# Optimization experiments

Hardware: AMD Instinct MI355X
Metric: run time of the kernel (lower is better)

The kernel has to match this reference:

```python
import jax, jax.numpy as jnp
import numpy as np

B, S, E = 2, 2049, 512
H, WIN = 8, 1024
D = E // H


def setup_inputs() -> dict:
    key = jax.random.key(0)
    ks = jax.random.split(key, 11)
    sc = 0.02
    return {
        "x": jax.random.normal(ks[0], (B, S, E), dtype=jnp.float32),
        "Wq": jax.random.normal(ks[1], (E, E), dtype=jnp.float32) * sc,
        "bq": jnp.zeros((E,), dtype=jnp.float32),
        "Wk": jax.random.normal(ks[2], (E, E), dtype=jnp.float32) * sc,
        "bk": jnp.zeros((E,), dtype=jnp.float32),
        "Wv": jax.random.normal(ks[3], (E, E), dtype=jnp.float32) * sc,
        "bv": jnp.zeros((E,), dtype=jnp.float32),
        "Wo": jax.random.normal(ks[4], (E, E), dtype=jnp.float32) * sc,
        "bo": jnp.zeros((E,), dtype=jnp.float32),
        "w_gate": jax.random.normal(ks[5], (2 * E,), dtype=jnp.float32) * sc,
        "b_gate": jnp.zeros((), dtype=jnp.float32),
    }


def reference(x, Wq, bq, Wk, bk, Wv, bv, Wo, bo, w_gate, b_gate):
    scale = D ** -0.5
    q_flat = x @ Wq + bq  # [B,S,E]
    k_flat = x @ Wk + bk
    v_flat = x @ Wv + bv
    q = q_flat.reshape(B, S, H, D).transpose(0, 2, 1, 3)  # [B,H,S,D]
    k = k_flat.reshape(B, S, H, D).transpose(0, 2, 1, 3)
    v = v_flat.reshape(B, S, H, D).transpose(0, 2, 1, 3)

    scores = jnp.einsum("bhqd,bhkd->bhqk", q, k) * scale  # [B,H,S,S]

    # Gaussian positional bias: -0.5*|i-j|^2/sigma^2, sigma = window/2
    pos = jnp.arange(S)
    dist = jnp.abs(pos[:, None] - pos[None, :]).astype(jnp.float32)
    sigma = WIN / 2.0
    bias = -0.5 * dist ** 2 / (sigma ** 2)  # [S,S]
    scores = scores + bias[None, None]

    # Pairwise gate: sigmoid(concat(q_i,k_j) @ w + b) == sigmoid(q_i.wq + k_j.wk + b)
    gq = q_flat @ w_gate[:E]       # [B,S]
    gk = k_flat @ w_gate[E:]       # [B,S]
    gates = jax.nn.sigmoid(gq[:, :, None] + gk[:, None, :] + b_gate)  # [B,S,S]
    scores = scores * gates[:, None]  # broadcast over heads

    local_mask = jnp.where(dist <= WIN, 0.0, -jnp.inf).astype(jnp.float32)
    scores = scores + local_mask[None, None]

    attn = jax.nn.softmax(scores, axis=-1)
    out = jnp.einsum("bhqk,bhkd->bhqd", attn, v)  # [B,H,S,D]
    out = out.transpose(0, 2, 1, 3).reshape(B, S, E)
    return out @ Wo + bo
```

## Files before the change

### kernel.cpp

```cpp
#include <hip/hip_runtime.h>
#include <cstdint>
#include <cstddef>

#define B_ 2
#define S_ 2049
#define E_ 512
#define H_ 8
#define WIN_ 1024
#define MROWS (B_*S_)
#define SP_ 2176
#define GBUFN 4104

typedef unsigned short ushort_t;
typedef __attribute__((ext_vector_type(8))) short bf16x8;
typedef __attribute__((ext_vector_type(4))) float f32x4;

#define MFMA16(a,b,c) __builtin_amdgcn_mfma_f32_16x16x32_bf16(a,b,c,0,0,0)

__device__ __forceinline__ ushort_t f2bf(float f) {
  unsigned int u = __float_as_uint(f);
  u += 0x7fffu + ((u >> 16) & 1u);
  return (ushort_t)(u >> 16);
}
__device__ __forceinline__ float bf2f(ushort_t h) {
  return __uint_as_float(((unsigned int)h) << 16);
}

__global__ __launch_bounds__(256) void convert_all_kernel(
    const float* __restrict__ x, const float* __restrict__ W0,
    const float* __restrict__ W1, const float* __restrict__ W2,
    const float* __restrict__ W3, ushort_t* __restrict__ xb,
    ushort_t* __restrict__ Wt_all, ushort_t* __restrict__ WoHi)
{
  __shared__ float tile[32][33];
  int bid = blockIdx.x;
  if (bid < 2049) {
    int idx = bid * 256 + threadIdx.x;
    float4 v = ((const float4*)x)[idx];
    ushort4 o;
    o.x = f2bf(v.x); o.y = f2bf(v.y); o.z = f2bf(v.z); o.w = f2bf(v.w);
    ((ushort4*)xb)[idx] = o;
    return;
  }
  int wid = bid - 2049;
  int z = wid >> 8, rem = wid & 255;
  const float* W = (z == 0) ? W0 : (z == 1) ? W1 : (z == 2) ? W2 : W3;
  int k0 = (rem >> 4) * 32, n0 = (rem & 15) * 32;
  int r = threadIdx.x >> 5, c = threadIdx.x & 31;
#pragma unroll
  for (int i = 0; i < 4; ++i) {
    int rr = r + i * 8;
    tile[rr][c] = W[(size_t)(k0 + rr) * E_ + n0 + c];
  }
  __syncthreads();
#pragma unroll
  for (int i = 0; i < 4; ++i) {
    int rr = r + i * 8;
    float v = tile[c][rr];
    size_t dst = (size_t)(n0 + rr) * E_ + k0 + c;
    if (z < 3) Wt_all[(size_t)z * E_ * E_ + dst] = f2bf(v);
    else       WoHi[dst] = f2bf(v);
  }
}

__global__ __launch_bounds__(256) void gemm_qkv_kernel(
    const ushort_t* __restrict__ xb, const ushort_t* __restrict__ Wt_all,
    const float* __restrict__ bq, const float* __restrict__ bk,
    const float* __restrict__ bv, const float* __restrict__ wg,
    ushort_t* __restrict__ qkb, ushort_t* __restrict__ vT,
    float* __restrict__ gq_acc, float* __restrict__ gk_acc)
{
  __shared__ __align__(16) ushort_t As[128][40];
  __shared__ __align__(16) ushort_t Bs[128][40];
  int tid = threadIdx.x;
  int lane = tid & 63, w = tid >> 6;
  int l15 = lane & 15, quad = lane >> 4;
  int wm = (w & 1) * 64, wn = (w >> 1) * 64;
  int z = blockIdx.z;
  const ushort_t* Wt = Wt_all + (size_t)z * E_ * E_;
  const float* bias = (z == 0) ? bq : (z == 1) ? bk : bv;
  int bm = blockIdx.x * 128, bn = blockIdx.y * 128;

  int ar = tid >> 1, ac = (tid & 1) * 16;
  int am = bm + ar; if (am >= MROWS) am = MROWS - 1;
  const ushort_t* ap = xb + (size_t)am * E_ + ac;
  const ushort_t* bp = Wt + (size_t)(bn + ar) * E_ + ac;

  const f32x4 fz = {0.f, 0.f, 0.f, 0.f};
  f32x4 acc[4][4];
#pragma unroll
  for (int mt = 0; mt < 4; ++mt)
#pragma unroll
    for (int nt = 0; nt < 4; ++nt) acc[mt][nt] = fz;

  int4 pa0 = *(const int4*)ap, pa1 = *(const int4*)(ap + 8);
  int4 pb0 = *(const int4*)bp, pb1 = *(const int4*)(bp + 8);

  for (int k0 = 0; k0 < E_; k0 += 32) {
    __syncthreads();
    int kn = (k0 + 32 < E_) ? (k0 + 32) : k0;
    int4 na0 = *(const int4*)(ap + kn), na1 = *(const int4*)(ap + kn + 8);
    int4 nb0 = *(const int4*)(bp + kn), nb1 = *(const int4*)(bp + kn + 8);
    *(int4*)&As[ar][ac] = pa0; *(int4*)&As[ar][ac + 8] = pa1;
    *(int4*)&Bs[ar][ac] = pb0; *(int4*)&Bs[ar][ac + 8] = pb1;
    __syncthreads();
    bf16x8 a[4], bfr[4];
#pragma unroll
    for (int mt = 0; mt < 4; ++mt) a[mt] = *(const bf16x8*)&As[wm + mt * 16 + l15][quad * 8];
#pragma unroll
    for (int nt = 0; nt < 4; ++nt) bfr[nt] = *(const bf16x8*)&Bs[wn + nt * 16 + l15][quad * 8];
#pragma unroll
    for (int mt = 0; mt < 4; ++mt)
#pragma unroll
      for (int nt = 0; nt < 4; ++nt)
        acc[mt][nt] = MFMA16(a[mt], bfr[nt], acc[mt][nt]);
    pa0 = na0; pa1 = na1; pb0 = nb0; pb1 = nb1;
  }

  float bb[4];
#pragma unroll
  for (int nt = 0; nt < 4; ++nt) bb[nt] = bias[bn + wn + nt * 16 + l15];

  if (z < 2) {
    ushort_t* C = qkb + (size_t)z * MROWS * E_;
#pragma unroll
    for (int mt = 0; mt < 4; ++mt)
#pragma unroll
      for (int nt = 0; nt < 4; ++nt)
#pragma unroll
        for (int r = 0; r < 4; ++r) {
          int m = bm + wm + mt * 16 + quad * 4 + r;
          if (m < MROWS)
            C[(size_t)m * E_ + bn + wn + nt * 16 + l15] = f2bf(acc[mt][nt][r] + bb[nt]);
        }
    const float* wgp = wg + (size_t)z * E_;
    float wv[4];
#pragma unroll
    for (int nt = 0; nt < 4; ++nt) wv[nt] = wgp[bn + wn + nt * 16 + l15];
    float* gacc = (z == 0) ? gq_acc : gk_acc;
#pragma unroll
    for (int mt = 0; mt < 4; ++mt)
#pragma unroll
      for (int r = 0; r < 4; ++r) {
        float s = 0.f;
#pragma unroll
        for (int nt = 0; nt < 4; ++nt) s = fmaf(acc[mt][nt][r] + bb[nt], wv[nt], s);
        s += __shfl_xor(s, 1, 16); s += __shfl_xor(s, 2, 16);
        s += __shfl_xor(s, 4, 16); s += __shfl_xor(s, 8, 16);
        int m = bm + wm + mt * 16 + quad * 4 + r;
        if (l15 == 0 && m < MROWS) atomicAdd(&gacc[m], s);
      }
  } else {
#pragma unroll
    for (int mt = 0; mt < 4; ++mt)
#pragma unroll
      for (int nt = 0; nt < 4; ++nt) {
        int dg = bn + wn + nt * 16 + l15;
        int h = dg >> 6, d = dg & 63;
#pragma unroll
        for (int r = 0; r < 4; ++r) {
          int m = bm + wm + mt * 16 + quad * 4 + r;
          if (m < MROWS) {
            int b = (m >= S_) ? 1 : 0;
            int i = m - b * S_;
            vT[((size_t)(b * H_ + h) * 64 + d) * SP_ + i] = f2bf(acc[mt][nt][r] + bb[nt]);
          }
        }
      }
  }
}

__global__ __launch_bounds__(256) void attn_kernel(
    const ushort_t* __restrict__ qb, const ushort_t* __restrict__ kb,
    const ushort_t* __restrict__ vT, const float* __restrict__ gq_raw,
    const float* __restrict__ gk_raw, const float* __restrict__ bgate,
    ushort_t* __restrict__ ahi, ushort_t* __restrict__ alo)
{
  __shared__ __align__(16) ushort_t Ks[64][72];
  __shared__ __align__(16) ushort_t Vt[64][72];
  __shared__ __align__(16) ushort_t Ps[4][16][72];
  __shared__ float lls[4][16];
  __shared__ float gbs[2176];

  int tid = threadIdx.x;
  int lane = tid & 63, w = tid >> 6;
  int l15 = lane & 15, quad = lane >> 4;

  int bh = blockIdx.x & 15;
  int qidx = blockIdx.x >> 4;
  int off = (qidx + 1) >> 1;
  int qt = 16 + ((qidx & 1) ? -off : off);
  int h = bh & 7, b = bh >> 3;
  int i0 = qt * 64;
  const float coef = -0.5f / (512.f * 512.f);

  int i = i0 + w * 16 + l15;
  int ic = (i < S_) ? i : S_ - 1;
  bf16x8 qf0 = *(const bf16x8*)&qb[((size_t)(b * S_ + ic)) * E_ + h * 64 + quad * 8];
  bf16x8 qf1 = *(const bf16x8*)&qb[((size_t)(b * S_ + ic)) * E_ + h * 64 + 32 + quad * 8];
#pragma unroll
  for (int e = 0; e < 8; ++e) {
    qf0[e] = (short)f2bf(bf2f((ushort_t)qf0[e]) * 0.125f);
    qf1[e] = (short)f2bf(bf2f((ushort_t)qf1[e]) * 0.125f);
  }
  float av = __expf(-(gq_raw[b * S_ + ic] + bgate[0]));
  float fdi = (i < S_) ? (float)i : -1e5f;

  int jlo = i0 - WIN_; if (jlo < 0) jlo = 0;
  int jt_lo = jlo >> 6;
  int jhi = i0 + 63 + WIN_; if (jhi > S_ - 1) jhi = S_ - 1;
  int jt_hi = jhi >> 6;
  int jbase = jt_lo << 6;
  int nwin = (jt_hi - jt_lo + 1) << 6;

  for (int tt = tid; tt < nwin; tt += 256) {
    int j = jbase + tt; int jc = (j < S_) ? j : S_ - 1;
    gbs[tt] = __expf(-gk_raw[b * S_ + jc]);
  }

  int srow = tid >> 2, scol = (tid & 3) * 16;
  const ushort_t* kb_base = kb + (size_t)b * S_ * E_ + h * 64 + scol;
  const ushort_t* vb_base = vT + ((size_t)(b * H_ + h) * 64 + srow) * SP_ + scol;

  int4 ka0, ka1, va0, va1;
  {
    int jc0 = jbase + srow; if (jc0 > S_ - 1) jc0 = S_ - 1;
    const int4* kp = (const int4*)(kb_base + (size_t)jc0 * E_);
    ka0 = kp[0]; ka1 = kp[1];
    const int4* vp = (const int4*)(vb_base + jbase);
    va0 = vp[0]; va1 = vp[1];
  }

  const f32x4 fz = {0.f, 0.f, 0.f, 0.f};
  f32x4 Ov[4] = {fz, fz, fz, fz};
  float l_run = 0.f;

  for (int jt = jt_lo; jt <= jt_hi; ++jt) {
    int j0 = jt << 6;
    __syncthreads();
    int jn = (jt < jt_hi) ? ((jt + 1) << 6) : j0;
    int jcn = jn + srow; if (jcn > S_ - 1) jcn = S_ - 1;
    const int4* kp = (const int4*)(kb_base + (size_t)jcn * E_);
    int4 nk0 = kp[0], nk1 = kp[1];
    const int4* vp = (const int4*)(vb_base + jn);
    int4 nv0 = vp[0], nv1 = vp[1];
    *(int4*)&Ks[srow][scol]     = ka0; *(int4*)&Ks[srow][scol + 8] = ka1;
    *(int4*)&Vt[srow][scol]     = va0; *(int4*)&Vt[srow][scol + 8] = va1;
    __syncthreads();

    f32x4 st[4];
#pragma unroll
    for (int nt = 0; nt < 4; ++nt) {
      bf16x8 kf0 = *(const bf16x8*)&Ks[nt * 16 + l15][quad * 8];
      bf16x8 kf1 = *(const bf16x8*)&Ks[nt * 16 + l15][32 + quad * 8];
      f32x4 s = MFMA16(kf0, qf0, fz);
      st[nt] = MFMA16(kf1, qf1, s);
    }

    bool full = ((j0 + 63 - i0) <= WIN_) && ((i0 + 63 - j0) <= WIN_)
                && (j0 + 63 < S_) && (i0 + 63 < S_);
    float ps = 0.f;
    float jq = (float)(j0 + quad * 4);
    if (full) {
#pragma unroll
      for (int nt = 0; nt < 4; ++nt) {
        f32x4 g4 = *(const f32x4*)&gbs[(j0 - jbase) + nt * 16 + quad * 4];
#pragma unroll
        for (int r = 0; r < 4; ++r) {
          float f = fdi - (jq + (float)(nt * 16 + r));
          float gate = __builtin_amdgcn_rcpf(fmaf(av, g4[r], 1.f));
          float p = __expf(fmaf(f * f, coef, st[nt][r]) * gate);
          st[nt][r] = p; ps += p;
        }
      }
    } else {
#pragma unroll
      for (int nt = 0; nt < 4; ++nt) {
        f32x4 g4 = *(const f32x4*)&gbs[(j0 - jbase) + nt * 16 + quad * 4];
#pragma unroll
        for (int r = 0; r < 4; ++r) {
          int j = j0 + nt * 16 + quad * 4 + r;
          float fj = (j < S_) ? (float)j : 1e5f;
          float f = fdi - fj;
          float gate = __builtin_amdgcn_rcpf(fmaf(av, g4[r], 1.f));
          float t = fmaf(f * f, coef, st[nt][r]) * gate;
          t = (__builtin_fabsf(f) <= 1024.f) ? t : -1e30f;
          float p = __expf(t);
          st[nt][r] = p; ps += p;
        }
      }
    }
    ps += __shfl_xor(ps, 16);
    ps += __shfl_xor(ps, 32);
    l_run += ps;

#pragma unroll
    for (int nt = 0; nt < 4; ++nt) {
      uint2 pk;
      pk.x = (unsigned int)f2bf(st[nt][0]) | ((unsigned int)f2bf(st[nt][1]) << 16);
      pk.y = (unsigned int)f2bf(st[nt][2]) | ((unsigned int)f2bf(st[nt][3]) << 16);
      *(uint2*)&Ps[w][l15][nt * 16 + quad * 4] = pk;
    }
    bf16x8 p0 = *(const bf16x8*)&Ps[w][l15][quad * 8];
    bf16x8 p1 = *(const bf16x8*)&Ps[w][l15][32 + quad * 8];
#pragma unroll
    for (int nt = 0; nt < 4; ++nt) {
      bf16x8 v0 = *(const bf16x8*)&Vt[nt * 16 + l15][quad * 8];
      bf16x8 v1 = *(const bf16x8*)&Vt[nt * 16 + l15][32 + quad * 8];
      Ov[nt] = MFMA16(p0, v0, Ov[nt]);
      Ov[nt] = MFMA16(p1, v1, Ov[nt]);
    }
    ka0 = nk0; ka1 = nk1; va0 = nv0; va1 = nv1;
  }

  if (lane < 16) lls[w][lane] = 1.f / l_run;
  f32x4 inv4 = *(const f32x4*)&lls[w][quad * 4];
#pragma unroll
  for (int r = 0; r < 4; ++r) {
    int irow = i0 + w * 16 + quad * 4 + r;
    if (irow < S_) {
#pragma unroll
      for (int nt = 0; nt < 4; ++nt) {
        float o = Ov[nt][r] * inv4[r];
        ushort_t hv = f2bf(o);
        size_t idx = ((size_t)(b * S_ + irow)) * E_ + h * 64 + nt * 16 + l15;
        ahi[idx] = hv;
        alo[idx] = f2bf(o - bf2f(hv));
      }
    }
  }
}

__global__ __launch_bounds__(256) void gemm_out_kernel(
    const ushort_t* __restrict__ Ahi, const ushort_t* __restrict__ Alo,
    const ushort_t* __restrict__ Whi, const float* __restrict__ bias,
    float* __restrict__ C)
{
  __shared__ __align__(16) ushort_t AsH[64][40];
  __shared__ __align__(16) ushort_t AsL[64][40];
  __shared__ __align__(16) ushort_t BsW[128][40];
  int tid = threadIdx.x;
  int lane = tid & 63, w = tid >> 6;
  int l15 = lane & 15, quad = lane >> 4;
  int wm = (w & 1) * 32, wn = (w >> 1) * 64;
  int bm = blockIdx.x * 64, bn = blockIdx.y * 128;

  int ar = tid >> 2, ac = (tid & 3) * 8;
  int am = bm + ar; if (am >= MROWS) am = MROWS - 1;
  const ushort_t* ahp = Ahi + (size_t)am * E_ + ac;
  const ushort_t* alp = Alo + (size_t)am * E_ + ac;
  int br = tid >> 1, bc = (tid & 1) * 16;
  const ushort_t* bp = Whi + (size_t)(bn + br) * E_ + bc;

  const f32x4 fz = {0.f, 0.f, 0.f, 0.f};
  f32x4 acc[2][4];
#pragma unroll
  for (int mt = 0; mt < 2; ++mt)
#pragma unroll
    for (int nt = 0; nt < 4; ++nt) acc[mt][nt] = fz;

  int4 ph = *(const int4*)ahp, pl = *(const int4*)alp;
  int4 pb0 = *(const int4*)bp, pb1 = *(const int4*)(bp + 8);

  for (int k0 = 0; k0 < E_; k0 += 32) {
    __syncthreads();
    int kn = (k0 + 32 < E_) ? (k0 + 32) : k0;
    int4 nh = *(const int4*)(ahp + kn), nl = *(const int4*)(alp + kn);
    int4 nb0 = *(const int4*)(bp + kn), nb1 = *(const int4*)(bp + kn + 8);
    *(int4*)&AsH[ar][ac] = ph;
    *(int4*)&AsL[ar][ac] = pl;
    *(int4*)&BsW[br][bc] = pb0; *(int4*)&BsW[br][bc + 8] = pb1;
    __syncthreads();
    bf16x8 ah[2], al[2], bw[4];
#pragma unroll
    for (int mt = 0; mt < 2; ++mt) {
      ah[mt] = *(const bf16x8*)&AsH[wm + mt * 16 + l15][quad * 8];
      al[mt] = *(const bf16x8*)&AsL[wm + mt * 16 + l15][quad * 8];
    }
#pragma unroll
    for (int nt = 0; nt < 4; ++nt) bw[nt] = *(const bf16x8*)&BsW[wn + nt * 16 + l15][quad * 8];
#pragma unroll
    for (int mt = 0; mt < 2; ++mt)
#pragma unroll
      for (int nt = 0; nt < 4; ++nt) {
        acc[mt][nt] = MFMA16(ah[mt], bw[nt], acc[mt][nt]);
        acc[mt][nt] = MFMA16(al[mt], bw[nt], acc[mt][nt]);
      }
    ph = nh; pl = nl; pb0 = nb0; pb1 = nb1;
  }
#pragma unroll
  for (int nt = 0; nt < 4; ++nt) {
    float bb = bias[bn + wn + nt * 16 + l15];
#pragma unroll
    for (int mt = 0; mt < 2; ++mt)
#pragma unroll
      for (int r = 0; r < 4; ++r) {
        int m = bm + wm + mt * 16 + quad * 4 + r;
        if (m < MROWS)
          C[(size_t)m * E_ + bn + wn + nt * 16 + l15] = acc[mt][nt][r] + bb;
      }
  }
}

extern "C" void kernel_launch(void* const* d_in, const int* in_sizes, int n_in,
                              void* d_out, int out_size, void* d_ws, size_t ws_size,
                              hipStream_t stream) {
  const float* x  = (const float*)d_in[0];
  const float* Wq = (const float*)d_in[1];
  const float* bq = (const float*)d_in[2];
  const float* Wk = (const float*)d_in[3];
  const float* bk = (const float*)d_in[4];
  const float* Wv = (const float*)d_in[5];
  const float* bv = (const float*)d_in[6];
  const float* Wo = (const float*)d_in[7];
  const float* bo = (const float*)d_in[8];
  const float* wg = (const float*)d_in[9];
  const float* bg = (const float*)d_in[10];

  char* p = (char*)d_ws;
  ushort_t* xb     = (ushort_t*)p; p += (size_t)MROWS * E_ * 2;
  ushort_t* Wt_all = (ushort_t*)p; p += (size_t)3 * E_ * E_ * 2;
  ushort_t* WoHi   = (ushort_t*)p; p += (size_t)E_ * E_ * 2;
  ushort_t* qkb    = (ushort_t*)p; p += (size_t)2 * MROWS * E_ * 2;
  ushort_t* vT     = (ushort_t*)p; p += (size_t)B_ * H_ * 64 * SP_ * 2;
  float*    gq_acc = (float*)p;    p += (size_t)GBUFN * 4;
  float*    gk_acc = (float*)p;    p += (size_t)GBUFN * 4;
  ushort_t* aHi    = (ushort_t*)p; p += (size_t)MROWS * E_ * 2;
  ushort_t* aLo    = (ushort_t*)p; p += (size_t)MROWS * E_ * 2;

  hipMemsetAsync(gq_acc, 0, 2 * (size_t)GBUFN * 4, stream);
  hipLaunchKernelGGL(convert_all_kernel, dim3(3073), dim3(256), 0, stream,
                     x, Wq, Wk, Wv, Wo, xb, Wt_all, WoHi);
  hipLaunchKernelGGL(gemm_qkv_kernel, dim3(33, 4, 3), dim3(256), 0, stream,
                     xb, Wt_all, bq, bk, bv, wg, qkb, vT, gq_acc, gk_acc);
  hipLaunchKernelGGL(attn_kernel, dim3(33 * 16), dim3(256), 0, stream,
                     qkb, qkb + (size_t)MROWS * E_, vT, gq_acc, gk_acc, bg, aHi, aLo);
  hipLaunchKernelGGL(gemm_out_kernel, dim3(65, 4), dim3(256), 0, stream,
                     aHi, aLo, WoHi, bo, (float*)d_out);
}
```

Measured before the change: 177.6 us.

## Split attention key range across two blocks, fuse x conversion into QKV GEMM

```diff
diff --git a/kernel.cpp b/kernel.cpp
--- a/kernel.cpp
+++ b/kernel.cpp
@@ -10,6 +10,8 @@
 #define MROWS (B_*S_)
 #define SP_ 2176
 #define GBUFN 4104
+#define HS_ (H_*S_)
+#define BHS_ (B_*H_*S_)
 
 typedef unsigned short ushort_t;
 typedef __attribute__((ext_vector_type(8))) short bf16x8;
@@ -26,26 +28,15 @@
   return __uint_as_float(((unsigned int)h) << 16);
 }
 
-__global__ __launch_bounds__(256) void convert_all_kernel(
-    const float* __restrict__ x, const float* __restrict__ W0,
-    const float* __restrict__ W1, const float* __restrict__ W2,
-    const float* __restrict__ W3, ushort_t* __restrict__ xb,
+__global__ __launch_bounds__(256) void convert_w_kernel(
+    const float* __restrict__ W0, const float* __restrict__ W1,
+    const float* __restrict__ W2, const float* __restrict__ W3,
     ushort_t* __restrict__ Wt_all, ushort_t* __restrict__ WoHi)
 {
   __shared__ float tile[32][33];
-  int bid = blockIdx.x;
-  if (bid < 2049) {
-    int idx = bid * 256 + threadIdx.x;
-    float4 v = ((const float4*)x)[idx];
-    ushort4 o;
-    o.x = f2bf(v.x); o.y = f2bf(v.y); o.z = f2bf(v.z); o.w = f2bf(v.w);
-    ((ushort4*)xb)[idx] = o;
-    return;
-  }
-  int wid = bid - 2049;
-  int z = wid >> 8, rem = wid & 255;
+  int z = blockIdx.z;
   const float* W = (z == 0) ? W0 : (z == 1) ? W1 : (z == 2) ? W2 : W3;
-  int k0 = (rem >> 4) * 32, n0 = (rem & 15) * 32;
+  int k0 = blockIdx.x * 32, n0 = blockIdx.y * 32;
   int r = threadIdx.x >> 5, c = threadIdx.x & 31;
 #pragma unroll
   for (int i = 0; i < 4; ++i) {
@@ -64,53 +55,57 @@
 }
 
 __global__ __launch_bounds__(256) void gemm_qkv_kernel(
-    const ushort_t* __restrict__ xb, const ushort_t* __restrict__ Wt_all,
+    const float* __restrict__ x, const ushort_t* __restrict__ Wt_all,
     const float* __restrict__ bq, const float* __restrict__ bk,
     const float* __restrict__ bv, const float* __restrict__ wg,
     ushort_t* __restrict__ qkb, ushort_t* __restrict__ vT,
     float* __restrict__ gq_acc, float* __restrict__ gk_acc)
 {
-  __shared__ __align__(16) ushort_t As[128][40];
+  __shared__ __align__(16) ushort_t As[64][40];
   __shared__ __align__(16) ushort_t Bs[128][40];
   int tid = threadIdx.x;
   int lane = tid & 63, w = tid >> 6;
   int l15 = lane & 15, quad = lane >> 4;
-  int wm = (w & 1) * 64, wn = (w >> 1) * 64;
+  int wm = (w & 1) * 32, wn = (w >> 1) * 64;
   int z = blockIdx.z;
   const ushort_t* Wt = Wt_all + (size_t)z * E_ * E_;
   const float* bias = (z == 0) ? bq : (z == 1) ? bk : bv;
-  int bm = blockIdx.x * 128, bn = blockIdx.y * 128;
-
-  int ar = tid >> 1, ac = (tid & 1) * 16;
+  int bm = blockIdx.x * 64, bn = blockIdx.y * 128;
+
+  int ar = tid >> 2, acq = (tid & 3) * 8;
   int am = bm + ar; if (am >= MROWS) am = MROWS - 1;
-  const ushort_t* ap = xb + (size_t)am * E_ + ac;
-  const ushort_t* bp = Wt + (size_t)(bn + ar) * E_ + ac;
+  const float* ap = x + (size_t)am * E_ + acq;
+  int br = tid >> 1, bcq = (tid & 1) * 16;
+  const ushort_t* bp = Wt + (size_t)(bn + br) * E_ + bcq;
 
   const f32x4 fz = {0.f, 0.f, 0.f, 0.f};
-  f32x4 acc[4][4];
-#pragma unroll
-  for (int mt = 0; mt < 4; ++mt)
+  f32x4 acc[2][4];
+#pragma unroll
+  for (int mt = 0; mt < 2; ++mt)
 #pragma unroll
     for (int nt = 0; nt < 4; ++nt) acc[mt][nt] = fz;
 
-  int4 pa0 = *(const int4*)ap, pa1 = *(const int4*)(ap + 8);
-  int4 pb0 = *(const int4*)bp, pb1 = *(const int4*)(bp + 8);
+  float4 pa0 = *(const float4*)ap, pa1 = *(const float4*)(ap + 4);
+  int4  pb0 = *(const int4*)bp,   pb1 = *(const int4*)(bp + 8);
 
   for (int k0 = 0; k0 < E_; k0 += 32) {
     __syncthreads();
     int kn = (k0 + 32 < E_) ? (k0 + 32) : k0;
-    int4 na0 = *(const int4*)(ap + kn), na1 = *(const int4*)(ap + kn + 8);
-    int4 nb0 = *(const int4*)(bp + kn), nb1 = *(const int4*)(bp + kn + 8);
-    *(int4*)&As[ar][ac] = pa0; *(int4*)&As[ar][ac + 8] = pa1;
-    *(int4*)&Bs[ar][ac] = pb0; *(int4*)&Bs[ar][ac + 8] = pb1;
-    __syncthreads();
-    bf16x8 a[4], bfr[4];
-#pragma unroll
-    for (int mt = 0; mt < 4; ++mt) a[mt] = *(const bf16x8*)&As[wm + mt * 16 + l15][quad * 8];
+    float4 na0 = *(const float4*)(ap + kn), na1 = *(const float4*)(ap + kn + 4);
+    int4  nb0 = *(const int4*)(bp + kn),   nb1 = *(const int4*)(bp + kn + 8);
+    union { int4 v; ushort_t u[8]; } cv;
+    cv.u[0] = f2bf(pa0.x); cv.u[1] = f2bf(pa0.y); cv.u[2] = f2bf(pa0.z); cv.u[3] = f2bf(pa0.w);
+    cv.u[4] = f2bf(pa1.x); cv.u[5] = f2bf(pa1.y); cv.u[6] = f2bf(pa1.z); cv.u[7] = f2bf(pa1.w);
+    *(int4*)&As[ar][acq] = cv.v;
+    *(int4*)&Bs[br][bcq] = pb0; *(int4*)&Bs[br][bcq + 8] = pb1;
+    __syncthreads();
+    bf16x8 a[2], bfr[4];
+#pragma unroll
+    for (int mt = 0; mt < 2; ++mt) a[mt] = *(const bf16x8*)&As[wm + mt * 16 + l15][quad * 8];
 #pragma unroll
     for (int nt = 0; nt < 4; ++nt) bfr[nt] = *(const bf16x8*)&Bs[wn + nt * 16 + l15][quad * 8];
 #pragma unroll
-    for (int mt = 0; mt < 4; ++mt)
+    for (int mt = 0; mt < 2; ++mt)
 #pragma unroll
       for (int nt = 0; nt < 4; ++nt)
         acc[mt][nt] = MFMA16(a[mt], bfr[nt], acc[mt][nt]);
@@ -124,7 +119,7 @@
   if (z < 2) {
     ushort_t* C = qkb + (size_t)z * MROWS * E_;
 #pragma unroll
-    for (int mt = 0; mt < 4; ++mt)
+    for (int mt = 0; mt < 2; ++mt)
 #pragma unroll
       for (int nt = 0; nt < 4; ++nt)
 #pragma unroll
@@ -139,7 +134,7 @@
     for (int nt = 0; nt < 4; ++nt) wv[nt] = wgp[bn + wn + nt * 16 + l15];
     float* gacc = (z == 0) ? gq_acc : gk_acc;
 #pragma unroll
-    for (int mt = 0; mt < 4; ++mt)
+    for (int mt = 0; mt < 2; ++mt)
 #pragma unroll
       for (int r = 0; r < 4; ++r) {
         float s = 0.f;
@@ -152,7 +147,7 @@
       }
   } else {
 #pragma unroll
-    for (int mt = 0; mt < 4; ++mt)
+    for (int mt = 0; mt < 2; ++mt)
 #pragma unroll
       for (int nt = 0; nt < 4; ++nt) {
         int dg = bn + wn + nt * 16 + l15;
@@ -174,22 +169,22 @@
     const ushort_t* __restrict__ qb, const ushort_t* __restrict__ kb,
     const ushort_t* __restrict__ vT, const float* __restrict__ gq_raw,
     const float* __restrict__ gk_raw, const float* __restrict__ bgate,
-    ushort_t* __restrict__ ahi, ushort_t* __restrict__ alo)
+    float* __restrict__ Opart, float* __restrict__ Lpart)
 {
   __shared__ __align__(16) ushort_t Ks[64][72];
   __shared__ __align__(16) ushort_t Vt[64][72];
   __shared__ __align__(16) ushort_t Ps[4][16][72];
-  __shared__ float lls[4][16];
-  __shared__ float gbs[2176];
+  __shared__ float gbs[1088];
 
   int tid = threadIdx.x;
   int lane = tid & 63, w = tid >> 6;
   int l15 = lane & 15, quad = lane >> 4;
 
-  int bh = blockIdx.x & 15;
-  int qidx = blockIdx.x >> 4;
+  int sub = blockIdx.x & 31;
+  int qidx = blockIdx.x >> 5;
   int off = (qidx + 1) >> 1;
   int qt = 16 + ((qidx & 1) ? -off : off);
+  int bh = sub & 15, half = sub >> 4;
   int h = bh & 7, b = bh >> 3;
   int i0 = qt * 64;
   const float coef = -0.5f / (512.f * 512.f);
@@ -210,8 +205,12 @@
   int jt_lo = jlo >> 6;
   int jhi = i0 + 63 + WIN_; if (jhi > S_ - 1) jhi = S_ - 1;
   int jt_hi = jhi >> 6;
-  int jbase = jt_lo << 6;
-  int nwin = (jt_hi - jt_lo + 1) << 6;
+  int L = jt_hi - jt_lo + 1;
+  int Lh = (L + 1) >> 1;
+  int myLo = half ? (jt_lo + Lh) : jt_lo;
+  int myHi = half ? jt_hi : (jt_lo + Lh - 1);
+  int jbase = myLo << 6;
+  int nwin = (myHi - myLo + 1) << 6;
 
   for (int tt = tid; tt < nwin; tt += 256) {
     int j = jbase + tt; int jc = (j < S_) ? j : S_ - 1;
@@ -235,17 +234,17 @@
   f32x4 Ov[4] = {fz, fz, fz, fz};
   float l_run = 0.f;
 
-  for (int jt = jt_lo; jt <= jt_hi; ++jt) {
+  for (int jt = myLo; jt <= myHi; ++jt) {
     int j0 = jt << 6;
     __syncthreads();
-    int jn = (jt < jt_hi) ? ((jt + 1) << 6) : j0;
+    int jn = (jt < myHi) ? ((jt + 1) << 6) : j0;
     int jcn = jn + srow; if (jcn > S_ - 1) jcn = S_ - 1;
     const int4* kp = (const int4*)(kb_base + (size_t)jcn * E_);
     int4 nk0 = kp[0], nk1 = kp[1];
     const int4* vp = (const int4*)(vb_base + jn);
     int4 nv0 = vp[0], nv1 = vp[1];
-    *(int4*)&Ks[srow][scol]     = ka0; *(int4*)&Ks[srow][scol + 8] = ka1;
-    *(int4*)&Vt[srow][scol]     = va0; *(int4*)&Vt[srow][scol + 8] = va1;
+    *(int4*)&Ks[srow][scol] = ka0; *(int4*)&Ks[srow][scol + 8] = ka1;
+    *(int4*)&Vt[srow][scol] = va0; *(int4*)&Vt[srow][scol + 8] = va1;
     __syncthreads();
 
     f32x4 st[4];
@@ -313,22 +312,49 @@
     ka0 = nk0; ka1 = nk1; va0 = nv0; va1 = nv1;
   }
 
-  if (lane < 16) lls[w][lane] = 1.f / l_run;
-  f32x4 inv4 = *(const f32x4*)&lls[w][quad * 4];
+  if (lane < 16) {
+    int irow = i0 + w * 16 + lane;
+    if (irow < S_)
+      Lpart[(size_t)half * BHS_ + (size_t)(b * H_ + h) * S_ + irow] = l_run;
+  }
 #pragma unroll
   for (int r = 0; r < 4; ++r) {
     int irow = i0 + w * 16 + quad * 4 + r;
     if (irow < S_) {
-#pragma unroll
-      for (int nt = 0; nt < 4; ++nt) {
-        float o = Ov[nt][r] * inv4[r];
-        ushort_t hv = f2bf(o);
-        size_t idx = ((size_t)(b * S_ + irow)) * E_ + h * 64 + nt * 16 + l15;
-        ahi[idx] = hv;
-        alo[idx] = f2bf(o - bf2f(hv));
-      }
-    }
-  }
+      size_t base = ((size_t)half * BHS_ + (size_t)(b * H_ + h) * S_ + irow) * (size_t)64;
+#pragma unroll
+      for (int nt = 0; nt < 4; ++nt)
+        Opart[base + nt * 16 + l15] = Ov[nt][r];
+    }
+  }
+}
+
+__global__ __launch_bounds__(256) void combine_kernel(
+    const float* __restrict__ Opart, const float* __restrict__ Lpart,
+    ushort_t* __restrict__ ahi, ushort_t* __restrict__ alo)
+{
+  int tid = threadIdx.x;
+  int gi = blockIdx.x * 16 + (tid >> 4);
+  int d4 = tid & 15;
+  int b = gi / HS_;
+  int rem = gi - b * HS_;
+  int h = rem / S_;
+  int i = rem - h * S_;
+  size_t p0 = (size_t)(b * H_ + h) * S_ + i;
+  size_t p1 = p0 + (size_t)BHS_;
+  float inv = __builtin_amdgcn_rcpf(Lpart[p0] + Lpart[p1]);
+  float4 o1 = *(const float4*)&Opart[p0 * 64 + d4 * 4];
+  float4 o2 = *(const float4*)&Opart[p1 * 64 + d4 * 4];
+  float o[4] = {(o1.x + o2.x) * inv, (o1.y + o2.y) * inv,
+                (o1.z + o2.z) * inv, (o1.w + o2.w) * inv};
+  ushort4 hi, lo;
+  hi.x = f2bf(o[0]); lo.x = f2bf(o[0] - bf2f(hi.x));
+  hi.y = f2bf(o[1]); lo.y = f2bf(o[1] - bf2f(hi.y));
+  hi.z = f2bf(o[2]); lo.z = f2bf(o[2] - bf2f(hi.z));
+  hi.w = f2bf(o[3]); lo.w = f2bf(o[3] - bf2f(hi.w));
+  size_t oidx = ((size_t)b * S_ + i) * E_ + h * 64 + d4 * 4;
+  *(ushort4*)&ahi[oidx] = hi;
+  *(ushort4*)&alo[oidx] = lo;
 }
 
 __global__ __launch_bounds__(256) void gemm_out_kernel(
@@ -338,67 +364,51 @@
 {
   __shared__ __align__(16) ushort_t AsH[64][40];
   __shared__ __align__(16) ushort_t AsL[64][40];
-  __shared__ __align__(16) ushort_t BsW[128][40];
+  __shared__ __align__(16) ushort_t BsW[64][40];
   int tid = threadIdx.x;
   int lane = tid & 63, w = tid >> 6;
   int l15 = lane & 15, quad = lane >> 4;
-  int wm = (w & 1) * 32, wn = (w >> 1) * 64;
-  int bm = blockIdx.x * 64, bn = blockIdx.y * 128;
-
-  int ar = tid >> 2, ac = (tid & 3) * 8;
-  int am = bm + ar; if (am >= MROWS) am = MROWS - 1;
-  const ushort_t* ahp = Ahi + (size_t)am * E_ + ac;
-  const ushort_t* alp = Alo + (size_t)am * E_ + ac;
-  int br = tid >> 1, bc = (tid & 1) * 16;
-  const ushort_t* bp = Whi + (size_t)(bn + br) * E_ + bc;
+  int bm = blockIdx.x * 64, bn = blockIdx.y * 64;
+  int sr = tid >> 2, sc = (tid & 3) * 8;
+  int am = bm + sr; if (am >= MROWS) am = MROWS - 1;
+  const ushort_t* ahp = Ahi + (size_t)am * E_ + sc;
+  const ushort_t* alp = Alo + (size_t)am * E_ + sc;
+  const ushort_t* bp  = Whi + (size_t)(bn + sr) * E_ + sc;
 
   const f32x4 fz = {0.f, 0.f, 0.f, 0.f};
-  f32x4 acc[2][4];
-#pragma unroll
-  for (int mt = 0; mt < 2; ++mt)
-#pragma unroll
-    for (int nt = 0; nt < 4; ++nt) acc[mt][nt] = fz;
-
-  int4 ph = *(const int4*)ahp, pl = *(const int4*)alp;
-  int4 pb0 = *(const int4*)bp, pb1 = *(const int4*)(bp + 8);
+  f32x4 acc[4] = {fz, fz, fz, fz};
+
+  int4 ph = *(const int4*)ahp, pl = *(const int4*)alp, pb = *(const int4*)bp;
 
   for (int k0 = 0; k0 < E_; k0 += 32) {
     __syncthreads();
     int kn = (k0 + 32 < E_) ? (k0 + 32) : k0;
-    int4 nh = *(const int4*)(ahp + kn), nl = *(const int4*)(alp + kn);
-    int4 nb0 = *(const int4*)(bp + kn), nb1 = *(const int4*)(bp + kn + 8);
-    *(int4*)&AsH[ar][ac] = ph;
-    *(int4*)&AsL[ar][ac] = pl;
-    *(int4*)&BsW[br][bc] = pb0; *(int4*)&BsW[br][bc + 8] = pb1;
-    __syncthreads();
-    bf16x8 ah[2], al[2], bw[4];
-#pragma unroll
-    for (int mt = 0; mt < 2; ++mt) {
-      ah[mt] = *(const bf16x8*)&AsH[wm + mt * 16 + l15][quad * 8];
-      al[mt] = *(const bf16x8*)&AsL[wm + mt * 16 + l15][quad * 8];
-    }
-#pragma unroll
-    for (int nt = 0; nt < 4; ++nt) bw[nt] = *(const bf16x8*)&BsW[wn + nt * 16 + l15][quad * 8];
-#pragma unroll
-    for (int mt = 0; mt < 2; ++mt)
-#pragma unroll
-      for (int nt = 0; nt < 4; ++nt) {
-        acc[mt][nt] = MFMA16(ah[mt], bw[nt], acc[mt][nt]);
-        acc[mt][nt] = MFMA16(al[mt], bw[nt], acc[mt][nt]);
-      }
-    ph = nh; pl = nl; pb0 = nb0; pb1 = nb1;
+    int4 nh = *(const int4*)(ahp + kn);
+    int4 nl = *(const int4*)(alp + kn);
+    int4 nb = *(const int4*)(bp + kn);
+    *(int4*)&AsH[sr][sc] = ph;
+    *(int4*)&AsL[sr][sc] = pl;
+    *(int4*)&BsW[sr][sc] = pb;
+    __syncthreads();
+    bf16x8 ah = *(const bf16x8*)&AsH[w * 16 + l15][quad * 8];
+    bf16x8 al = *(const bf16x8*)&AsL[w * 16 + l15][quad * 8];
+#pragma unroll
+    for (int nt = 0; nt < 4; ++nt) {
+      bf16x8 bw = *(const bf16x8*)&BsW[nt * 16 + l15][quad * 8];
+      acc[nt] = MFMA16(ah, bw, acc[nt]);
+      acc[nt] = MFMA16(al, bw, acc[nt]);
+    }
+    ph = nh; pl = nl; pb = nb;
   }
 #pragma unroll
   for (int nt = 0; nt < 4; ++nt) {
-    float bb = bias[bn + wn + nt * 16 + l15];
-#pragma unroll
-    for (int mt = 0; mt < 2; ++mt)
-#pragma unroll
-      for (int r = 0; r < 4; ++r) {
-        int m = bm + wm + mt * 16 + quad * 4 + r;
-        if (m < MROWS)
-          C[(size_t)m * E_ + bn + wn + nt * 16 + l15] = acc[mt][nt][r] + bb;
-      }
+    float bb = bias[bn + nt * 16 + l15];
+#pragma unroll
+    for (int r = 0; r < 4; ++r) {
+      int m = bm + w * 16 + quad * 4 + r;
+      if (m < MROWS)
+        C[(size_t)m * E_ + bn + nt * 16 + l15] = acc[nt][r] + bb;
+    }
   }
 }
 
@@ -418,23 +428,27 @@
   const float* bg = (const float*)d_in[10];
 
   char* p = (char*)d_ws;
-  ushort_t* xb     = (ushort_t*)p; p += (size_t)MROWS * E_ * 2;
   ushort_t* Wt_all = (ushort_t*)p; p += (size_t)3 * E_ * E_ * 2;
   ushort_t* WoHi   = (ushort_t*)p; p += (size_t)E_ * E_ * 2;
   ushort_t* qkb    = (ushort_t*)p; p += (size_t)2 * MROWS * E_ * 2;
   ushort_t* vT     = (ushort_t*)p; p += (size_t)B_ * H_ * 64 * SP_ * 2;
   float*    gq_acc = (float*)p;    p += (size_t)GBUFN * 4;
   float*    gk_acc = (float*)p;    p += (size_t)GBUFN * 4;
+  float*    Opart  = (float*)p;    p += (size_t)2 * BHS_ * 64 * 4;
+  float*    Lpart  = (float*)p;    p += (size_t)2 * BHS_ * 4;
   ushort_t* aHi    = (ushort_t*)p; p += (size_t)MROWS * E_ * 2;
   ushort_t* aLo    = (ushort_t*)p; p += (size_t)MROWS * E_ * 2;
 
   hipMemsetAsync(gq_acc, 0, 2 * (size_t)GBUFN * 4, stream);
-  hipLaunchKernelGGL(convert_all_kernel, dim3(3073), dim3(256), 0, stream,
-                     x, Wq, Wk, Wv, Wo, xb, Wt_all, WoHi);
-  hipLaunchKernelGGL(gemm_qkv_kernel, dim3(33, 4, 3), dim3(256), 0, stream,
-                     xb, Wt_all, bq, bk, bv, wg, qkb, vT, gq_acc, gk_acc);
-  hipLaunchKernelGGL(attn_kernel, dim3(33 * 16), dim3(256), 0, stream,
-                     qkb, qkb + (size_t)MROWS * E_, vT, gq_acc, gk_acc, bg, aHi, aLo);
-  hipLaunchKernelGGL(gemm_out_kernel, dim3(65, 4), dim3(256), 0, stream,
+  hipLaunchKernelGGL(convert_w_kernel, dim3(16, 16, 4), dim3(256), 0, stream,
+                     Wq, Wk, Wv, Wo, Wt_all, WoHi);
+  hipLaunchKernelGGL(gemm_qkv_kernel, dim3(65, 4, 3), dim3(256), 0, stream,
+                     x, Wt_all, bq, bk, bv, wg, qkb, vT, gq_acc, gk_acc);
+  hipLaunchKernelGGL(attn_kernel, dim3(33 * 32), dim3(256), 0, stream,
+                     qkb, qkb + (size_t)MROWS * E_, vT, gq_acc, gk_acc, bg,
+                     Opart, Lpart);
+  hipLaunchKernelGGL(combine_kernel, dim3(2049), dim3(256), 0, stream,
+                     Opart, Lpart, aHi, aLo);
+  hipLaunchKernelGGL(gemm_out_kernel, dim3(65, 8), dim3(256), 0, stream,
                      aHi, aLo, WoHi, bo, (float*)d_out);
 }
```

Result: no change. 175.6 us (-1.2%).
